# Kernel tuning notes

Hardware: AMD Instinct MI355X
Metric: run time of the kernel (lower is better)

The kernel has to match this reference:

```python
import jax, jax.numpy as jnp
import numpy as np

NUM_GRAPHS = 512

def setup_inputs() -> dict:
    key = jax.random.key(0)
    ks = jax.random.split(key, 8)
    N, E, SD = 50000, 800000, 128
    x_ids = jax.random.randint(ks[0], (N,), 0, 1340)
    edge_index = jax.random.randint(ks[1], (2, E), 0, N)
    batch = jnp.sort(jax.random.randint(ks[2], (N,), 0, NUM_GRAPHS))
    emb = jax.random.normal(ks[3], (1340, SD), dtype=jnp.float32) * 0.1
    W1 = jax.random.normal(ks[4], (SD, 2 * SD), dtype=jnp.float32) * 0.1
    b1 = jnp.zeros((2 * SD,), dtype=jnp.float32)
    W2 = jax.random.normal(ks[5], (2 * SD, 41), dtype=jnp.float32) * 0.1
    b2 = jnp.zeros((41,), dtype=jnp.float32)
    return {"x_ids": x_ids, "edge_index": edge_index, "batch": batch,
            "emb": emb, "W1": W1, "b1": b1, "W2": W2, "b2": b2}

def _gcn_conv(x, src, dst, W, b, num_nodes):
    # x: [N, Fin] -> [N, Fout]; GCN: add self-loops, deg^-1/2 norm, transform, aggregate
    deg = jax.ops.segment_sum(jnp.ones_like(dst, dtype=x.dtype), dst, num_segments=num_nodes)
    dinv = jnp.where(deg > 0, jax.lax.rsqrt(jnp.where(deg > 0, deg, 1.0)), 0.0)
    norm = dinv[src] * dinv[dst]               # [E+N]
    h = x @ W                                  # [N, Fout]
    msg = h[src] * norm[:, None]               # [E+N, Fout] gather (memory-bound)
    out = jax.ops.segment_sum(msg, dst, num_segments=num_nodes)
    return out + b

def reference(x_ids, edge_index, batch, emb, W1, b1, W2, b2):
    N = x_ids.shape[0]
    loops = jnp.arange(N, dtype=edge_index.dtype)
    src = jnp.concatenate([edge_index[0], loops])
    dst = jnp.concatenate([edge_index[1], loops])
    x = emb[x_ids]                                   # embedding lookup [N, SD]
    x = _gcn_conv(x, src, dst, W1, b1, N)
    x = jax.nn.relu(x)                               # dropout is identity in eval mode
    x = _gcn_conv(x, src, dst, W2, b2, N)
    return jax.ops.segment_sum(x, batch, num_segments=NUM_GRAPHS)  # [512, 41]
```

## Files before the change

### kernel.cpp

```cpp
#include <hip/hip_runtime.h>

#define N_NODES 50000
#define N_EDGES 800000
#define N_TOT   850000
#define SD 128
#define HD 256
#define OD 41
#define ODP 48
#define NG 512
#define NB 128
#define NPB 391
#define BCAP 8192

typedef __attribute__((ext_vector_type(8))) short bh8;
typedef __attribute__((ext_vector_type(4))) float f4;
typedef unsigned long long u64;

__device__ inline unsigned short f2bf(float x) {
  unsigned u = __float_as_uint(x);
  unsigned r = u + 0x7fff + ((u >> 16) & 1);
  return (unsigned short)(r >> 16);
}
__device__ inline float bf2f(unsigned short s) {
  return __uint_as_float(((unsigned)s) << 16);
}
__device__ inline float bflo(unsigned e) { return __uint_as_float(e << 16); }
__device__ inline float bfhi(unsigned e) { return __uint_as_float(e & 0xffff0000u); }
__device__ inline unsigned pk2(float lo, float hi) {
  return (unsigned)f2bf(lo) | ((unsigned)f2bf(hi) << 16);
}

__device__ inline unsigned rec_xid(u64 r)  { return ((unsigned)r) >> 16; }
__device__ inline unsigned rec_src(u64 r)  { return ((unsigned)r) & 0xFFFFu; }
__device__ inline float    rec_nrm(u64 r)  { return __uint_as_float((unsigned)(r >> 32) & 0xFFFF0000u); }

__global__ __launch_bounds__(256) void init_kernel(const float* __restrict__ emb,
    const float* __restrict__ W1, const float* __restrict__ W2,
    const int* __restrict__ batch,
    unsigned short* __restrict__ embb, unsigned short* __restrict__ w1f,
    unsigned short* __restrict__ w2f, float4* __restrict__ curB4,
    float4* __restrict__ out4, int* __restrict__ gstart) {
  int tid = blockIdx.x * 256 + threadIdx.x;
  if (tid < 1340 * SD) { embb[tid] = f2bf(emb[tid]); return; }
  int u = tid - 1340 * SD;
  if (u < 4096) {
    int lane = u & 63, frag = u >> 6;
    int ks = frag >> 4, cf = frag & 15;
    int col = cf * 16 + (lane & 15);
    #pragma unroll
    for (int j = 0; j < 8; ++j) {
      int k = ks * 32 + ((lane >> 4) << 3) + j;
      w1f[u * 8 + j] = f2bf(W1[k * HD + col]);
    }
    return;
  }
  u -= 4096;
  if (u < 1536) {
    int lane = u & 63, frag = u >> 6;
    int ks = frag / 3, cf = frag % 3;
    int col = cf * 16 + (lane & 15);
    #pragma unroll
    for (int j = 0; j < 8; ++j) {
      int k = ks * 32 + ((lane >> 4) << 3) + j;
      w2f[u * 8 + j] = (col < OD) ? f2bf(W2[k * OD + col]) : (unsigned short)0;
    }
    return;
  }
  u -= 1536;
  float4 z = make_float4(0.f, 0.f, 0.f, 0.f);
  if (u < 32) { curB4[u] = z; return; }
  u -= 32;
  if (u < 5248) { out4[u] = z; return; }
  u -= 5248;
  if (u < N_NODES) {
    int i = u;
    if (i == 0) {
      for (int g = 0; g <= batch[0]; ++g) gstart[g] = 0;
    } else {
      int bp = batch[i - 1], bn = batch[i];
      for (int g = bp + 1; g <= bn; ++g) gstart[g] = i;
    }
    if (i == N_NODES - 1) {
      for (int g = batch[i] + 1; g <= NG; ++g) gstart[g] = N_NODES;
    }
  }
}

__global__ __launch_bounds__(256) void passA_kernel(const int* __restrict__ ei,
    const int* __restrict__ x_ids, int* __restrict__ curB, u64* __restrict__ stage) {
  __shared__ int lcur[NB];
  __shared__ int base[NB];
  int t = threadIdx.x;
  if (t < NB) lcur[t] = 0;
  __syncthreads();
  u64 pay[16];
  int loc[16];
  int e0 = blockIdx.x * 4096;
  #pragma unroll
  for (int j = 0; j < 16; ++j) {
    int e = e0 + j * 256 + t;
    loc[j] = -1;
    if (e < N_TOT) {
      int s, d;
      if (e < N_EDGES) { s = ei[e]; d = ei[N_EDGES + e]; }
      else             { s = d = e - N_EDGES; }
      int b = d / NPB;
      int lofs = atomicAdd(&lcur[b], 1);
      loc[j] = (b << 13) | lofs;
      pay[j] = ((u64)(unsigned)x_ids[s] << 32) | ((u64)(unsigned)d << 16) | (u64)(unsigned)s;
    }
  }
  __syncthreads();
  if (t < NB) base[t] = atomicAdd(&curB[t], lcur[t]);
  __syncthreads();
  #pragma unroll
  for (int j = 0; j < 16; ++j) {
    if (loc[j] >= 0) {
      int b = loc[j] >> 13, lofs = loc[j] & 8191;
      stage[(size_t)b * BCAP + base[b] + lofs] = pay[j];
    }
  }
}

__global__ __launch_bounds__(256) void countscan_kernel(const int* __restrict__ curB,
    const u64* __restrict__ stage, int* __restrict__ off, float* __restrict__ dinv) {
  __shared__ int cl[NPB];
  __shared__ int sc[512];
  __shared__ int bs[NB];
  int t = threadIdx.x, k = blockIdx.x;
  for (int l = t; l < NPB; l += 256) cl[l] = 0;
  if (t < NB) bs[t] = curB[t];
  __syncthreads();
  for (int s = 1; s < NB; s <<= 1) {
    int a = (t < NB && t >= s) ? bs[t - s] : 0;
    __syncthreads();
    if (t < NB) bs[t] += a;
    __syncthreads();
  }
  int base = (k == 0) ? 0 : bs[k - 1];
  int nbk = curB[k];
  const u64* st = stage + (size_t)k * BCAP;
  for (int i = t; i < nbk; i += 256) {
    int d = (int)((st[i] >> 16) & 0xFFFFu);
    atomicAdd(&cl[d - k * NPB], 1);
  }
  __syncthreads();
  sc[t]       = (t < NPB)       ? cl[t]       : 0;
  sc[t + 256] = (t + 256 < NPB) ? cl[t + 256] : 0;
  __syncthreads();
  for (int s = 1; s < 512; s <<= 1) {
    int a0 = (t >= s) ? sc[t - s] : 0;
    int a1 = (t + 256 >= s) ? sc[t + 256 - s] : 0;
    __syncthreads();
    sc[t] += a0; sc[t + 256] += a1;
    __syncthreads();
  }
  int n0 = k * NPB;
  int nn = (n0 + NPB <= N_NODES) ? NPB : (N_NODES - n0);
  for (int l = t; l < nn; l += 256) {
    int v = cl[l];
    off[n0 + l] = base + sc[l] - v;
    dinv[n0 + l] = rsqrtf((float)v);
  }
  if (k == 0 && t == 0) off[N_NODES] = N_TOT;
}

__global__ __launch_bounds__(256) void passB_kernel(const int* __restrict__ curB,
    const u64* __restrict__ stage, const int* __restrict__ off,
    const float* __restrict__ dinv, u64* __restrict__ rec) {
  __shared__ int lcur[NPB];
  __shared__ int loff[NPB];
  int t = threadIdx.x, k = blockIdx.x;
  int n0 = k * NPB;
  int nn = (n0 + NPB <= N_NODES) ? NPB : (N_NODES - n0);
  for (int l = t; l < nn; l += 256) { lcur[l] = 0; loff[l] = off[n0 + l]; }
  __syncthreads();
  int nbk = curB[k];
  const u64* st = stage + (size_t)k * BCAP;
  for (int i = t; i < nbk; i += 256) {
    u64 r = st[i];
    int s   = (int)(r & 0xFFFFu);
    int d   = (int)((r >> 16) & 0xFFFFu);
    int xid = (int)((r >> 32) & 0xFFFFu);
    float nrm = dinv[s] * dinv[d];
    int ld = d - n0;
    int p = loff[ld] + atomicAdd(&lcur[ld], 1);
    rec[p] = ((u64)f2bf(nrm) << 48) | ((u64)(unsigned)xid << 16) | (u64)(unsigned)s;
  }
}

__global__ __launch_bounds__(256) void agg1w_kernel(const int* __restrict__ off,
    const u64* __restrict__ rec, const uint4* __restrict__ emb16,
    uint4* __restrict__ agg16) {
  int lane = threadIdx.x & 63;
  int node = __builtin_amdgcn_readfirstlane(blockIdx.x * 4 + (threadIdx.x >> 6));
  int beg = off[node], end = off[node + 1];
  int eslot = lane >> 4, fgrp = lane & 15;
  float a[8];
  #pragma unroll
  for (int j = 0; j < 8; ++j) a[j] = 0.f;
  int i = beg;
  for (; i + 16 <= end; i += 16) {
    u64 r0 = rec[i + eslot];
    u64 r1 = rec[i + 4 + eslot];
    u64 r2 = rec[i + 8 + eslot];
    u64 r3 = rec[i + 12 + eslot];
    uint4 v0 = emb16[rec_xid(r0) * 16 + fgrp];
    uint4 v1 = emb16[rec_xid(r1) * 16 + fgrp];
    uint4 v2 = emb16[rec_xid(r2) * 16 + fgrp];
    uint4 v3 = emb16[rec_xid(r3) * 16 + fgrp];
    float n0 = rec_nrm(r0), n1 = rec_nrm(r1), n2 = rec_nrm(r2), n3 = rec_nrm(r3);
    a[0] += n0 * bflo(v0.x); a[1] += n0 * bfhi(v0.x);
    a[2] += n0 * bflo(v0.y); a[3] += n0 * bfhi(v0.y);
    a[4] += n0 * bflo(v0.z); a[5] += n0 * bfhi(v0.z);
    a[6] += n0 * bflo(v0.w); a[7] += n0 * bfhi(v0.w);
    a[0] += n1 * bflo(v1.x); a[1] += n1 * bfhi(v1.x);
    a[2] += n1 * bflo(v1.y); a[3] += n1 * bfhi(v1.y);
    a[4] += n1 * bflo(v1.z); a[5] += n1 * bfhi(v1.z);
    a[6] += n1 * bflo(v1.w); a[7] += n1 * bfhi(v1.w);
    a[0] += n2 * bflo(v2.x); a[1] += n2 * bfhi(v2.x);
    a[2] += n2 * bflo(v2.y); a[3] += n2 * bfhi(v2.y);
    a[4] += n2 * bflo(v2.z); a[5] += n2 * bfhi(v2.z);
    a[6] += n2 * bflo(v2.w); a[7] += n2 * bfhi(v2.w);
    a[0] += n3 * bflo(v3.x); a[1] += n3 * bfhi(v3.x);
    a[2] += n3 * bflo(v3.y); a[3] += n3 * bfhi(v3.y);
    a[4] += n3 * bflo(v3.z); a[5] += n3 * bfhi(v3.z);
    a[6] += n3 * bflo(v3.w); a[7] += n3 * bfhi(v3.w);
  }
  for (; i + 8 <= end; i += 8) {
    u64 rA = rec[i + eslot];
    u64 rB = rec[i + 4 + eslot];
    uint4 vA = emb16[rec_xid(rA) * 16 + fgrp];
    uint4 vB = emb16[rec_xid(rB) * 16 + fgrp];
    float nA = rec_nrm(rA), nB = rec_nrm(rB);
    a[0] += nA * bflo(vA.x); a[1] += nA * bfhi(vA.x);
    a[2] += nA * bflo(vA.y); a[3] += nA * bfhi(vA.y);
    a[4] += nA * bflo(vA.z); a[5] += nA * bfhi(vA.z);
    a[6] += nA * bflo(vA.w); a[7] += nA * bfhi(vA.w);
    a[0] += nB * bflo(vB.x); a[1] += nB * bfhi(vB.x);
    a[2] += nB * bflo(vB.y); a[3] += nB * bfhi(vB.y);
    a[4] += nB * bflo(vB.z); a[5] += nB * bfhi(vB.z);
    a[6] += nB * bflo(vB.w); a[7] += nB * bfhi(vB.w);
  }
  for (; i < end; i += 4) {
    int idx = i + eslot;
    bool val = idx < end;
    u64 r = rec[val ? idx : (end - 1)];
    uint4 v = emb16[rec_xid(r) * 16 + fgrp];
    float n = val ? rec_nrm(r) : 0.f;
    a[0] += n * bflo(v.x); a[1] += n * bfhi(v.x);
    a[2] += n * bflo(v.y); a[3] += n * bfhi(v.y);
    a[4] += n * bflo(v.z); a[5] += n * bfhi(v.z);
    a[6] += n * bflo(v.w); a[7] += n * bfhi(v.w);
  }
  #pragma unroll
  for (int j = 0; j < 8; ++j) {
    a[j] += __shfl_xor(a[j], 16);
    a[j] += __shfl_xor(a[j], 32);
  }
  if (lane < 16) {
    uint4 o;
    o.x = pk2(a[0], a[1]); o.y = pk2(a[2], a[3]);
    o.z = pk2(a[4], a[5]); o.w = pk2(a[6], a[7]);
    agg16[(size_t)node * 16 + fgrp] = o;
  }
}

__global__ __launch_bounds__(256) void gemm12_mfma(const unsigned short* __restrict__ agg1,
    const bh8* __restrict__ w1f, const float* __restrict__ b1,
    const bh8* __restrict__ w2f, unsigned short* __restrict__ h2b) {
  __shared__ char raw[32768];
  int t = threadIdx.x, lane = t & 63, wave = t >> 6;
  int row0 = blockIdx.x * 64;
  #pragma unroll
  for (int k = 0; k < 4; ++k) {
    int idx = k * 256 + t;
    int r = idx >> 4, cc = idx & 15;
    int4 v = make_int4(0, 0, 0, 0);
    if (row0 + r < N_NODES)
      v = *(const int4*)((const char*)agg1 + (size_t)(row0 + r) * 256 + cc * 16);
    *(int4*)(raw + ((r * 256 + cc * 16) ^ ((r & 15) << 4))) = v;
  }
  bh8 bf1[4][4];
  #pragma unroll
  for (int cf = 0; cf < 4; ++cf)
    #pragma unroll
    for (int ks = 0; ks < 4; ++ks)
      bf1[cf][ks] = w1f[(ks * 16 + wave * 4 + cf) * 64 + lane];
  f4 acc[4][4];
  #pragma unroll
  for (int rf = 0; rf < 4; ++rf)
    #pragma unroll
    for (int cf = 0; cf < 4; ++cf)
      acc[rf][cf] = (f4){0.f, 0.f, 0.f, 0.f};
  __syncthreads();
  #pragma unroll
  for (int ks = 0; ks < 4; ++ks) {
    bh8 a[4];
    #pragma unroll
    for (int rf = 0; rf < 4; ++rf) {
      int r = rf * 16 + (lane & 15);
      int byte = (r * 256 + ks * 64 + ((lane >> 4) << 4)) ^ ((r & 15) << 4);
      a[rf] = *(const bh8*)(raw + byte);
    }
    #pragma unroll
    for (int rf = 0; rf < 4; ++rf)
      #pragma unroll
      for (int cf = 0; cf < 4; ++cf)
        acc[rf][cf] = __builtin_amdgcn_mfma_f32_16x16x32_bf16(a[rf], bf1[cf][ks], acc[rf][cf], 0, 0, 0);
  }
  __syncthreads();
  #pragma unroll
  for (int cf = 0; cf < 4; ++cf) {
    int col = wave * 64 + cf * 16 + (lane & 15);
    float bias = b1[col];
    #pragma unroll
    for (int rf = 0; rf < 4; ++rf)
      #pragma unroll
      for (int j = 0; j < 4; ++j) {
        int r = rf * 16 + ((lane >> 4) << 2) + j;
        unsigned short v = f2bf(fmaxf(acc[rf][cf][j] + bias, 0.f));
        *(unsigned short*)(raw + ((r * 512 + col * 2) ^ ((r & 15) << 4))) = v;
      }
  }
  bh8 bf2[3][8];
  #pragma unroll
  for (int cf = 0; cf < 3; ++cf)
    #pragma unroll
    for (int ks = 0; ks < 8; ++ks)
      bf2[cf][ks] = w2f[(ks * 3 + cf) * 64 + lane];
  f4 acc2[3];
  #pragma unroll
  for (int cf = 0; cf < 3; ++cf) acc2[cf] = (f4){0.f, 0.f, 0.f, 0.f};
  __syncthreads();
  int r2 = wave * 16 + (lane & 15);
  #pragma unroll
  for (int ks = 0; ks < 8; ++ks) {
    int byte = (r2 * 512 + ks * 64 + ((lane >> 4) << 4)) ^ ((r2 & 15) << 4);
    bh8 a = *(const bh8*)(raw + byte);
    #pragma unroll
    for (int cf = 0; cf < 3; ++cf)
      acc2[cf] = __builtin_amdgcn_mfma_f32_16x16x32_bf16(a, bf2[cf][ks], acc2[cf], 0, 0, 0);
  }
  #pragma unroll
  for (int cf = 0; cf < 3; ++cf) {
    int col = cf * 16 + (lane & 15);
    #pragma unroll
    for (int j = 0; j < 4; ++j) {
      int rg = row0 + wave * 16 + ((lane >> 4) << 2) + j;
      if (rg < N_NODES)
        h2b[(size_t)rg * ODP + col] = f2bf(acc2[cf][j]);
    }
  }
}

__global__ __launch_bounds__(256) void pool2_kernel(const int* __restrict__ gstart,
    const int* __restrict__ off, const u64* __restrict__ rec,
    const unsigned short* __restrict__ h2b, const float* __restrict__ b2,
    float* __restrict__ out) {
  __shared__ float red[4][60][8];
  int g = blockIdx.x >> 3, c = blockIdx.x & 7;
  int t = threadIdx.x, lane = t & 63, wv = t >> 6;
  int n0 = gstart[g], n1 = gstart[g + 1];
  int e0 = off[n0], e1 = off[n1];
  int len = e1 - e0;
  int c0 = e0 + ((len * c) >> 3);
  int c1 = e0 + ((len * (c + 1)) >> 3);
  int clen = c1 - c0;
  int w0 = c0 + ((clen * wv) >> 2);
  int w1 = c0 + ((clen * (wv + 1)) >> 2);
  bool live = lane < 60;
  int eslot = live ? lane / 6 : 0;
  int fgrp  = live ? lane - (lane / 6) * 6 : 0;
  float a[8];
  #pragma unroll
  for (int j = 0; j < 8; ++j) a[j] = 0.f;
  int i = w0;
  for (; i + 20 <= w1; i += 20) {
    u64 rA = rec[i + eslot];
    u64 rB = rec[i + 10 + eslot];
    uint4 vA = *(const uint4*)(h2b + (size_t)rec_src(rA) * ODP + fgrp * 8);
    uint4 vB = *(const uint4*)(h2b + (size_t)rec_src(rB) * ODP + fgrp * 8);
    float nA = live ? rec_nrm(rA) : 0.f;
    float nB = live ? rec_nrm(rB) : 0.f;
    a[0] += nA * bflo(vA.x); a[1] += nA * bfhi(vA.x);
    a[2] += nA * bflo(vA.y); a[3] += nA * bfhi(vA.y);
    a[4] += nA * bflo(vA.z); a[5] += nA * bfhi(vA.z);
    a[6] += nA * bflo(vA.w); a[7] += nA * bfhi(vA.w);
    a[0] += nB * bflo(vB.x); a[1] += nB * bfhi(vB.x);
    a[2] += nB * bflo(vB.y); a[3] += nB * bfhi(vB.y);
    a[4] += nB * bflo(vB.z); a[5] += nB * bfhi(vB.z);
    a[6] += nB * bflo(vB.w); a[7] += nB * bfhi(vB.w);
  }
  for (; i + 10 <= w1; i += 10) {
    u64 r = rec[i + eslot];
    uint4 v = *(const uint4*)(h2b + (size_t)rec_src(r) * ODP + fgrp * 8);
    float n = live ? rec_nrm(r) : 0.f;
    a[0] += n * bflo(v.x); a[1] += n * bfhi(v.x);
    a[2] += n * bflo(v.y); a[3] += n * bfhi(v.y);
    a[4] += n * bflo(v.z); a[5] += n * bfhi(v.z);
    a[6] += n * bflo(v.w); a[7] += n * bfhi(v.w);
  }
  if (i < w1) {
    int idx = i + eslot;
    bool val = live && idx < w1;
    u64 r = rec[val ? idx : w0];
    uint4 v = *(const uint4*)(h2b + (size_t)rec_src(r) * ODP + fgrp * 8);
    float n = val ? rec_nrm(r) : 0.f;
    a[0] += n * bflo(v.x); a[1] += n * bfhi(v.x);
    a[2] += n * bflo(v.y); a[3] += n * bfhi(v.y);
    a[4] += n * bflo(v.z); a[5] += n * bfhi(v.z);
    a[6] += n * bflo(v.w); a[7] += n * bfhi(v.w);
  }
  if (live) {
    #pragma unroll
    for (int j = 0; j < 8; ++j) red[wv][lane][j] = a[j];
  }
  __syncthreads();
  if (t < 48) {
    int fg = t >> 3, j = t & 7;
    float s = 0.f;
    #pragma unroll
    for (int w = 0; w < 4; ++w)
      #pragma unroll
      for (int e = 0; e < 10; ++e)
        s += red[w][e * 6 + fg][j];
    if (t < OD) {
      if (c == 0) s += (float)(n1 - n0) * b2[t];
      unsafeAtomicAdd(&out[g * OD + t], s);
    }
  }
}

extern "C" void kernel_launch(void* const* d_in, const int* in_sizes, int n_in,
                              void* d_out, int out_size, void* d_ws, size_t ws_size,
                              hipStream_t stream) {
  const int*   x_ids = (const int*)d_in[0];
  const int*   ei    = (const int*)d_in[1];
  const int*   batch = (const int*)d_in[2];
  const float* emb   = (const float*)d_in[3];
  const float* W1    = (const float*)d_in[4];
  const float* b1    = (const float*)d_in[5];
  const float* W2    = (const float*)d_in[6];
  const float* b2    = (const float*)d_in[7];
  float* out = (float*)d_out;
  char* ws = (char*)d_ws;

  int*            curB   = (int*)           (ws + 0);
  float*          dinv   = (float*)         (ws + 4096);
  int*            off    = (int*)           (ws + 208896);
  int*            gstart = (int*)           (ws + 413696);
  unsigned short* embb   = (unsigned short*)(ws + 1048576);
  unsigned short* w1f    = (unsigned short*)(ws + 1441792);
  unsigned short* w2f    = (unsigned short*)(ws + 1507328);
  u64*            rec    = (u64*)           (ws + 2097152);
  u64*            stage  = (u64*)           (ws + 9437184);
  unsigned short* agg1   = (unsigned short*)(ws + 18874368);
  unsigned short* h2b    = (unsigned short*)(ws + 33554432);

  init_kernel <<<908, 256, 0, stream>>>(emb, W1, W2, batch, embb, w1f, w2f,
                                        (float4*)curB, (float4*)out, gstart);
  passA_kernel<<<208, 256, 0, stream>>>(ei, x_ids, curB, stage);
  countscan_kernel<<<NB, 256, 0, stream>>>(curB, stage, off, dinv);
  passB_kernel<<<NB,  256, 0, stream>>>(curB, stage, off, dinv, rec);

  agg1w_kernel<<<12500, 256, 0, stream>>>(off, rec, (const uint4*)embb, (uint4*)agg1);
  gemm12_mfma <<<782,   256, 0, stream>>>(agg1, (const bh8*)w1f, b1, (const bh8*)w2f, h2b);
  pool2_kernel<<<4096,  256, 0, stream>>>(gstart, off, rec, h2b, b2, out);
}
```

Measured before the change: 101.8 us.

## Fuse layer-1 neighbor aggregation into the MFMA GEMM kernel via shared memory

```diff
diff --git a/kernel.cpp b/kernel.cpp
--- a/kernel.cpp
+++ b/kernel.cpp
@@ -189,98 +189,91 @@
   }
 }
 
-__global__ __launch_bounds__(256) void agg1w_kernel(const int* __restrict__ off,
+__global__ __launch_bounds__(256) void fused12_kernel(const int* __restrict__ off,
     const u64* __restrict__ rec, const uint4* __restrict__ emb16,
-    uint4* __restrict__ agg16) {
-  int lane = threadIdx.x & 63;
-  int node = __builtin_amdgcn_readfirstlane(blockIdx.x * 4 + (threadIdx.x >> 6));
-  int beg = off[node], end = off[node + 1];
-  int eslot = lane >> 4, fgrp = lane & 15;
-  float a[8];
-  #pragma unroll
-  for (int j = 0; j < 8; ++j) a[j] = 0.f;
-  int i = beg;
-  for (; i + 16 <= end; i += 16) {
-    u64 r0 = rec[i + eslot];
-    u64 r1 = rec[i + 4 + eslot];
-    u64 r2 = rec[i + 8 + eslot];
-    u64 r3 = rec[i + 12 + eslot];
-    uint4 v0 = emb16[rec_xid(r0) * 16 + fgrp];
-    uint4 v1 = emb16[rec_xid(r1) * 16 + fgrp];
-    uint4 v2 = emb16[rec_xid(r2) * 16 + fgrp];
-    uint4 v3 = emb16[rec_xid(r3) * 16 + fgrp];
-    float n0 = rec_nrm(r0), n1 = rec_nrm(r1), n2 = rec_nrm(r2), n3 = rec_nrm(r3);
-    a[0] += n0 * bflo(v0.x); a[1] += n0 * bfhi(v0.x);
-    a[2] += n0 * bflo(v0.y); a[3] += n0 * bfhi(v0.y);
-    a[4] += n0 * bflo(v0.z); a[5] += n0 * bfhi(v0.z);
-    a[6] += n0 * bflo(v0.w); a[7] += n0 * bfhi(v0.w);
-    a[0] += n1 * bflo(v1.x); a[1] += n1 * bfhi(v1.x);
-    a[2] += n1 * bflo(v1.y); a[3] += n1 * bfhi(v1.y);
-    a[4] += n1 * bflo(v1.z); a[5] += n1 * bfhi(v1.z);
-    a[6] += n1 * bflo(v1.w); a[7] += n1 * bfhi(v1.w);
-    a[0] += n2 * bflo(v2.x); a[1] += n2 * bfhi(v2.x);
-    a[2] += n2 * bflo(v2.y); a[3] += n2 * bfhi(v2.y);
-    a[4] += n2 * bflo(v2.z); a[5] += n2 * bfhi(v2.z);
-    a[6] += n2 * bflo(v2.w); a[7] += n2 * bfhi(v2.w);
-    a[0] += n3 * bflo(v3.x); a[1] += n3 * bfhi(v3.x);
-    a[2] += n3 * bflo(v3.y); a[3] += n3 * bfhi(v3.y);
-    a[4] += n3 * bflo(v3.z); a[5] += n3 * bfhi(v3.z);
-    a[6] += n3 * bflo(v3.w); a[7] += n3 * bfhi(v3.w);
-  }
-  for (; i + 8 <= end; i += 8) {
-    u64 rA = rec[i + eslot];
-    u64 rB = rec[i + 4 + eslot];
-    uint4 vA = emb16[rec_xid(rA) * 16 + fgrp];
-    uint4 vB = emb16[rec_xid(rB) * 16 + fgrp];
-    float nA = rec_nrm(rA), nB = rec_nrm(rB);
-    a[0] += nA * bflo(vA.x); a[1] += nA * bfhi(vA.x);
-    a[2] += nA * bflo(vA.y); a[3] += nA * bfhi(vA.y);
-    a[4] += nA * bflo(vA.z); a[5] += nA * bfhi(vA.z);
-    a[6] += nA * bflo(vA.w); a[7] += nA * bfhi(vA.w);
-    a[0] += nB * bflo(vB.x); a[1] += nB * bfhi(vB.x);
-    a[2] += nB * bflo(vB.y); a[3] += nB * bfhi(vB.y);
-    a[4] += nB * bflo(vB.z); a[5] += nB * bfhi(vB.z);
-    a[6] += nB * bflo(vB.w); a[7] += nB * bfhi(vB.w);
-  }
-  for (; i < end; i += 4) {
-    int idx = i + eslot;
-    bool val = idx < end;
-    u64 r = rec[val ? idx : (end - 1)];
-    uint4 v = emb16[rec_xid(r) * 16 + fgrp];
-    float n = val ? rec_nrm(r) : 0.f;
-    a[0] += n * bflo(v.x); a[1] += n * bfhi(v.x);
-    a[2] += n * bflo(v.y); a[3] += n * bfhi(v.y);
-    a[4] += n * bflo(v.z); a[5] += n * bfhi(v.z);
-    a[6] += n * bflo(v.w); a[7] += n * bfhi(v.w);
-  }
-  #pragma unroll
-  for (int j = 0; j < 8; ++j) {
-    a[j] += __shfl_xor(a[j], 16);
-    a[j] += __shfl_xor(a[j], 32);
-  }
-  if (lane < 16) {
-    uint4 o;
-    o.x = pk2(a[0], a[1]); o.y = pk2(a[2], a[3]);
-    o.z = pk2(a[4], a[5]); o.w = pk2(a[6], a[7]);
-    agg16[(size_t)node * 16 + fgrp] = o;
-  }
-}
-
-__global__ __launch_bounds__(256) void gemm12_mfma(const unsigned short* __restrict__ agg1,
     const bh8* __restrict__ w1f, const float* __restrict__ b1,
     const bh8* __restrict__ w2f, unsigned short* __restrict__ h2b) {
   __shared__ char raw[32768];
   int t = threadIdx.x, lane = t & 63, wave = t >> 6;
   int row0 = blockIdx.x * 64;
-  #pragma unroll
-  for (int k = 0; k < 4; ++k) {
-    int idx = k * 256 + t;
-    int r = idx >> 4, cc = idx & 15;
-    int4 v = make_int4(0, 0, 0, 0);
-    if (row0 + r < N_NODES)
-      v = *(const int4*)((const char*)agg1 + (size_t)(row0 + r) * 256 + cc * 16);
-    *(int4*)(raw + ((r * 256 + cc * 16) ^ ((r & 15) << 4))) = v;
-  }
+  int eslot = lane >> 4, fgrp = lane & 15;
+
+  for (int ln = 0; ln < 16; ++ln) {
+    int r = wave * 16 + ln;
+    int node = row0 + r;
+    float a[8];
+    #pragma unroll
+    for (int j = 0; j < 8; ++j) a[j] = 0.f;
+    if (node < N_NODES) {
+      int beg = off[node], end = off[node + 1];
+      int i = beg;
+      for (; i + 16 <= end; i += 16) {
+        u64 r0 = rec[i + eslot];
+        u64 r1 = rec[i + 4 + eslot];
+        u64 r2 = rec[i + 8 + eslot];
+        u64 r3 = rec[i + 12 + eslot];
+        uint4 v0 = emb16[rec_xid(r0) * 16 + fgrp];
+        uint4 v1 = emb16[rec_xid(r1) * 16 + fgrp];
+        uint4 v2 = emb16[rec_xid(r2) * 16 + fgrp];
+        uint4 v3 = emb16[rec_xid(r3) * 16 + fgrp];
+        float n0 = rec_nrm(r0), n1 = rec_nrm(r1), n2 = rec_nrm(r2), n3 = rec_nrm(r3);
+        a[0] += n0 * bflo(v0.x); a[1] += n0 * bfhi(v0.x);
+        a[2] += n0 * bflo(v0.y); a[3] += n0 * bfhi(v0.y);
+        a[4] += n0 * bflo(v0.z); a[5] += n0 * bfhi(v0.z);
+        a[6] += n0 * bflo(v0.w); a[7] += n0 * bfhi(v0.w);
+        a[0] += n1 * bflo(v1.x); a[1] += n1 * bfhi(v1.x);
+        a[2] += n1 * bflo(v1.y); a[3] += n1 * bfhi(v1.y);
+        a[4] += n1 * bflo(v1.z); a[5] += n1 * bfhi(v1.z);
+        a[6] += n1 * bflo(v1.w); a[7] += n1 * bfhi(v1.w);
+        a[0] += n2 * bflo(v2.x); a[1] += n2 * bfhi(v2.x);
+        a[2] += n2 * bflo(v2.y); a[3] += n2 * bfhi(v2.y);
+        a[4] += n2 * bflo(v2.z); a[5] += n2 * bfhi(v2.z);
+        a[6] += n2 * bflo(v2.w); a[7] += n2 * bfhi(v2.w);
+        a[0] += n3 * bflo(v3.x); a[1] += n3 * bfhi(v3.x);
+        a[2] += n3 * bflo(v3.y); a[3] += n3 * bfhi(v3.y);
+        a[4] += n3 * bflo(v3.z); a[5] += n3 * bfhi(v3.z);
+        a[6] += n3 * bflo(v3.w); a[7] += n3 * bfhi(v3.w);
+      }
+      for (; i + 8 <= end; i += 8) {
+        u64 rA = rec[i + eslot];
+        u64 rB = rec[i + 4 + eslot];
+        uint4 vA = emb16[rec_xid(rA) * 16 + fgrp];
+        uint4 vB = emb16[rec_xid(rB) * 16 + fgrp];
+        float nA = rec_nrm(rA), nB = rec_nrm(rB);
+        a[0] += nA * bflo(vA.x); a[1] += nA * bfhi(vA.x);
+        a[2] += nA * bflo(vA.y); a[3] += nA * bfhi(vA.y);
+        a[4] += nA * bflo(vA.z); a[5] += nA * bfhi(vA.z);
+        a[6] += nA * bflo(vA.w); a[7] += nA * bfhi(vA.w);
+        a[0] += nB * bflo(vB.x); a[1] += nB * bfhi(vB.x);
+        a[2] += nB * bflo(vB.y); a[3] += nB * bfhi(vB.y);
+        a[4] += nB * bflo(vB.z); a[5] += nB * bfhi(vB.z);
+        a[6] += nB * bflo(vB.w); a[7] += nB * bfhi(vB.w);
+      }
+      for (; i < end; i += 4) {
+        int idx = i + eslot;
+        bool val = idx < end;
+        u64 r4 = rec[val ? idx : (end - 1)];
+        uint4 v = emb16[rec_xid(r4) * 16 + fgrp];
+        float n = val ? rec_nrm(r4) : 0.f;
+        a[0] += n * bflo(v.x); a[1] += n * bfhi(v.x);
+        a[2] += n * bflo(v.y); a[3] += n * bfhi(v.y);
+        a[4] += n * bflo(v.z); a[5] += n * bfhi(v.z);
+        a[6] += n * bflo(v.w); a[7] += n * bfhi(v.w);
+      }
+    }
+    #pragma unroll
+    for (int j = 0; j < 8; ++j) {
+      a[j] += __shfl_xor(a[j], 16);
+      a[j] += __shfl_xor(a[j], 32);
+    }
+    if (lane < 16) {
+      uint4 o;
+      o.x = pk2(a[0], a[1]); o.y = pk2(a[2], a[3]);
+      o.z = pk2(a[4], a[5]); o.w = pk2(a[6], a[7]);
+      *(uint4*)(raw + ((r * 256 + fgrp * 16) ^ ((r & 15) << 4))) = o;
+    }
+  }
+
   bh8 bf1[4][4];
   #pragma unroll
   for (int cf = 0; cf < 4; ++cf)
@@ -455,8 +448,7 @@
   unsigned short* w2f    = (unsigned short*)(ws + 1507328);
   u64*            rec    = (u64*)           (ws + 2097152);
   u64*            stage  = (u64*)           (ws + 9437184);
-  unsigned short* agg1   = (unsigned short*)(ws + 18874368);
-  unsigned short* h2b    = (unsigned short*)(ws + 33554432);
+  unsigned short* h2b    = (unsigned short*)(ws + 18874368);
 
   init_kernel <<<908, 256, 0, stream>>>(emb, W1, W2, batch, embb, w1f, w2f,
                                         (float4*)curB, (float4*)out, gstart);
@@ -464,7 +456,7 @@
   countscan_kernel<<<NB, 256, 0, stream>>>(curB, stage, off, dinv);
   passB_kernel<<<NB,  256, 0, stream>>>(curB, stage, off, dinv, rec);
 
-  agg1w_kernel<<<12500, 256, 0, stream>>>(off, rec, (const uint4*)embb, (uint4*)agg1);
-  gemm12_mfma <<<782,   256, 0, stream>>>(agg1, (const bh8*)w1f, b1, (const bh8*)w2f, h2b);
-  pool2_kernel<<<4096,  256, 0, stream>>>(gstart, off, rec, h2b, b2, out);
-}
+  fused12_kernel<<<782, 256, 0, stream>>>(off, rec, (const uint4*)embb,
+                                          (const bh8*)w1f, b1, (const bh8*)w2f, h2b);
+  pool2_kernel<<<4096, 256, 0, stream>>>(gstart, off, rec, h2b, b2, out);
+}
```

After: 128.0 us. 25.7% more time.
